# Kernel tuning notes

Hardware: AMD Instinct MI355X
Metric: run time of the kernel (lower is better)

Reference implementation:

```python
import jax, jax.numpy as jnp
import numpy as np

H = 768      # hidden size
F = 3072     # FFN intermediate (4*H)
E = 8        # num experts
K = 2        # top_k
B, S = 2, 2048


def setup_inputs() -> dict:
    key = jax.random.key(0)
    ks = jax.random.split(key, 6)
    scale_in = 1.0 / np.sqrt(H)
    scale_mid = 1.0 / np.sqrt(F)
    return {
        "x": jax.random.normal(ks[0], (B, S, H), dtype=jnp.float32),
        "gate_w": jax.random.normal(ks[1], (H, E), dtype=jnp.float32) * scale_in,
        "W1": jax.random.normal(ks[2], (E, H, F), dtype=jnp.float32) * scale_in,
        "b1": jnp.zeros((E, F), dtype=jnp.float32),
        "W2": jax.random.normal(ks[3], (E, F, H), dtype=jnp.float32) * scale_mid,
        "b2": jnp.zeros((E, H), dtype=jnp.float32),
    }


def reference(x, gate_w, W1, b1, W2, b2):
    """MoE FFN: top-k router -> per-expert FFN -> weighted combine.

    Faithful to the torch module: router logits = x @ gate_w (no bias),
    softmax over the top-k logits only, each expert is a dense FFN
    (Linear -> GELU -> Linear), output = sum_k w_k * expert_{idx_k}(x).
    Expressed densely: combine weights are scattered into a [T, E] matrix
    (zero for unselected experts), so running every expert on every token
    and contracting with the combine matrix yields identical math.
    """
    batch, seq_len, hidden = x.shape
    xf = x.reshape(-1, hidden)                       # [T, H]
    T = xf.shape[0]

    logits = xf @ gate_w                             # [T, E]
    top_w, top_idx = jax.lax.top_k(logits, K)        # [T, K]
    top_w = jax.nn.softmax(top_w, axis=-1)

    # scatter top-k softmax weights into dense [T, E] combine matrix
    comb = jnp.zeros((T, E), dtype=x.dtype).at[
        jnp.arange(T)[:, None], top_idx
    ].add(top_w)

    # all experts on all tokens (zero combine weight kills unselected)
    h = jnp.einsum('th,ehf->etf', xf, W1) + b1[:, None, :]   # [E, T, F]
    h = jax.nn.gelu(h)
    y = jnp.einsum('etf,efh->eth', h, W2) + b2[:, None, :]   # [E, T, H]

    out = jnp.einsum('te,eth->th', comb, y)                  # [T, H]
    return out.reshape(batch, seq_len, hidden)
```

## Files before the change

### kernel.cpp

```cpp
#include <hip/hip_runtime.h>

#define H 768
#define F 3072
#define NE 8
#define T 4096
#define NA 8192
#define TP 10240
#define NRB2 40
#define NRB1 80

typedef unsigned short ushort_t;
typedef __attribute__((ext_vector_type(8))) short bfx8;
typedef __attribute__((ext_vector_type(4))) float fx4;
typedef __attribute__((address_space(3))) const ushort_t lus;

__device__ __forceinline__ ushort_t f2bf(float f) {
    union { float f; unsigned u; } v; v.f = f;
    unsigned u = v.u;
    unsigned r = (u + 0x7fffu + ((u >> 16) & 1u)) >> 16;
    return (ushort_t)r;
}

__device__ __forceinline__ float gelu_tanh(float x) {
    const float c = 0.7978845608028654f;
    float z = c * (x + 0.044715f * x * x * x);
    float t = 1.0f - 2.0f / (__expf(2.0f * z) + 1.0f);
    return 0.5f * x * (1.0f + t);
}

__device__ __forceinline__ void g2l16(const void* g, void* l) {
    __builtin_amdgcn_global_load_lds(
        (__attribute__((address_space(1))) void*)g,
        (__attribute__((address_space(3))) void*)l, 16, 0, 0);
}

__device__ __forceinline__ bfx8 dsr128(lus* p) {
    bfx8 r;
    asm volatile("ds_read_b128 %0, %1" : "=v"(r) : "v"(p));
    return r;
}

#define WAITV6 asm volatile("s_waitcnt vmcnt(6)" ::: "memory")
#define WAITV0 asm volatile("s_waitcnt vmcnt(0)" ::: "memory")
#define LGKM8  asm volatile("s_waitcnt lgkmcnt(8)" ::: "memory")
#define LGKM0  asm volatile("s_waitcnt lgkmcnt(0)" ::: "memory")
#define SBAR   asm volatile("s_barrier" ::: "memory")
#define SCHED0 __builtin_amdgcn_sched_barrier(0)
#define PRIO1  __builtin_amdgcn_s_setprio(1)
#define PRIO0  __builtin_amdgcn_s_setprio(0)

__global__ void router_k(const float* __restrict__ x, const float* __restrict__ gw,
                         int* __restrict__ tidx, float* __restrict__ twgt) {
    int t = blockIdx.x * 4 + (threadIdx.x >> 6);
    int lane = threadIdx.x & 63;
    const float* xr = x + (size_t)t * H;
    float acc[NE];
#pragma unroll
    for (int e = 0; e < NE; ++e) acc[e] = 0.f;
    for (int h = lane; h < H; h += 64) {
        float xv = xr[h];
        const float* g = gw + h * NE;
#pragma unroll
        for (int e = 0; e < NE; ++e) acc[e] += xv * g[e];
    }
#pragma unroll
    for (int off = 32; off > 0; off >>= 1) {
#pragma unroll
        for (int e = 0; e < NE; ++e) acc[e] += __shfl_down(acc[e], off);
    }
    if (lane == 0) {
        float l0 = -1e30f, l1 = -1e30f; int i0 = 0, i1 = 0;
#pragma unroll
        for (int e = 0; e < NE; ++e) {
            float v = acc[e];
            if (v > l0) { l1 = l0; i1 = i0; l0 = v; i0 = e; }
            else if (v > l1) { l1 = v; i1 = e; }
        }
        float w0 = 1.f / (1.f + __expf(l1 - l0));
        tidx[t * 2] = i0; tidx[t * 2 + 1] = i1;
        twgt[t * 2] = w0; twgt[t * 2 + 1] = 1.f - w0;
    }
}

__global__ void init_k(int* counts, int* tos) {
    int i = blockIdx.x * 256 + threadIdx.x;
    if (i < NE) counts[i] = 0;
    if (i < TP) tos[i] = -1;
}

__global__ void count_k(const int* __restrict__ tidx, int* counts) {
    int i = blockIdx.x * 256 + threadIdx.x;
    if (i < NA) atomicAdd(&counts[tidx[i]], 1);
}

__global__ void offsets_k(const int* __restrict__ counts, int* cursor,
                          int* rbe2, int* rbs2, int* rbe1, int* rbs1) {
    int off = 0, rb2 = 0, rb1 = 0;
    for (int e = 0; e < NE; ++e) {
        cursor[e] = off;
        int nrb = (counts[e] + 255) / 256;
        for (int j = 0; j < nrb; ++j) {
            rbe2[rb2] = e; rbs2[rb2] = off + j * 256; ++rb2;
            rbe1[rb1] = e; rbs1[rb1] = off + j * 256; ++rb1;
            rbe1[rb1] = e; rbs1[rb1] = off + j * 256 + 128; ++rb1;
        }
        off += nrb * 256;
    }
    for (; rb2 < NRB2; ++rb2) rbe2[rb2] = -1;
    for (; rb1 < NRB1; ++rb1) rbe1[rb1] = -1;
}

__global__ void scatter_k(const int* __restrict__ tidx, int* cursor,
                          int* __restrict__ tos, int* __restrict__ aslot) {
    int i = blockIdx.x * 256 + threadIdx.x;
    if (i < NA) {
        int e = tidx[i];
        int slot = atomicAdd(&cursor[e], 1);
        tos[slot] = i >> 1;
        aslot[i] = slot;
    }
}

__global__ void gather_k(const float* __restrict__ x, const int* __restrict__ tos,
                         ushort_t* __restrict__ xg) {
    int i = blockIdx.x * 256 + threadIdx.x;
    int slot = i / (H / 8);
    int j = i % (H / 8);
    int tok = tos[slot];
    ushort_t v[8];
    if (tok < 0) {
#pragma unroll
        for (int q = 0; q < 8; ++q) v[q] = 0;
    } else {
        const float* src = x + (size_t)tok * H + j * 8;
#pragma unroll
        for (int q = 0; q < 8; ++q) v[q] = f2bf(src[q]);
    }
    *(bfx8*)&xg[(size_t)slot * H + j * 8] = *(const bfx8*)v;
}

__global__ void transpose_cast_k(const float* __restrict__ src, ushort_t* __restrict__ dst,
                                 int R, int C) {
    int e = blockIdx.z;
    src += (size_t)e * R * C;
    dst += (size_t)e * R * C;
    int c0 = blockIdx.x * 64, r0 = blockIdx.y * 64;
    __shared__ float tile[64][65];
    int tid = threadIdx.x;
    int cc = tid & 63, rr = tid >> 6;
#pragma unroll
    for (int rep = 0; rep < 16; ++rep) {
        int r = rep * 4 + rr;
        tile[r][cc] = src[(size_t)(r0 + r) * C + c0 + cc];
    }
    __syncthreads();
#pragma unroll
    for (int rep = 0; rep < 16; ++rep) {
        int c = rep * 4 + rr;
        dst[(size_t)(c0 + c) * R + r0 + cc] = f2bf(tile[cc][c]);
    }
}

template <int WM, int WN, int DO_GELU>
__global__ __launch_bounds__(512, 2)
void gemm_tile_k(const ushort_t* __restrict__ A, const ushort_t* __restrict__ Bt,
                 const float* __restrict__ bias, void* __restrict__ Cout,
                 const int* __restrict__ rbe, const int* __restrict__ rbs,
                 int K, int N, int ncb) {
    constexpr int BM = WM * 64, BN = WN * 64;
    constexpr int UA = BM / 64, UB = BN / 64;
    constexpr int BUFS = (BM + BN) * 64;

    int nwg = gridDim.x, bid = blockIdx.x;
    int wgid = (bid & 7) * (nwg >> 3) + (bid >> 3);
    int rb = wgid / ncb, cb = wgid % ncb;
    int e = rbe[rb];
    if (e < 0) return;
    int slot0 = rbs[rb];

    __shared__ __align__(16) ushort_t lds[3 * BUFS];

    int tid = threadIdx.x, lane = tid & 63, wid = tid >> 6;
    int wm = wid / WN, wn = wid % WN;
    int l15 = lane & 15, qh = lane >> 4, sw = l15 & 7;

    const ushort_t* Ab = A + (size_t)slot0 * K;
    const ushort_t* Bb = Bt + ((size_t)e * N + cb * BN) * K;

    int j = tid >> 3, q = tid & 7;
    int cs = (q ^ (j & 7)) * 8;
    int ldsw = wid * 512;
    const ushort_t* aSrc = Ab + (size_t)j * K + cs;
    const ushort_t* bSrc = Bb + (size_t)j * K + cs;

    int ch0 = ((0 * 4 + qh) ^ sw) << 3;
    int ch1 = ((1 * 4 + qh) ^ sw) << 3;
    int abase = (wm * 64 + l15) * 64;
    int bbase = BM * 64 + (wn * 64 + l15) * 64;

#define STAGE_T(NB, KT) do { \
    _Pragma("unroll") for (int u = 0; u < UA; ++u) \
        g2l16(aSrc + (size_t)u * 64 * K + (KT) * 64, \
              &lds[(NB) * BUFS + u * 4096 + ldsw]); \
    _Pragma("unroll") for (int u = 0; u < UB; ++u) \
        g2l16(bSrc + (size_t)u * 64 * K + (KT) * 64, \
              &lds[(NB) * BUFS + BM * 64 + u * 4096 + ldsw]); \
} while (0)

    fx4 acc[4][4];
#pragma unroll
    for (int m = 0; m < 4; ++m)
#pragma unroll
        for (int n = 0; n < 4; ++n) acc[m][n] = (fx4){0.f, 0.f, 0.f, 0.f};
    bfx8 a0[4], a1[4], b0v[4], b1v[4];

    int NT = K >> 6;
    STAGE_T(0, 0);
    STAGE_T(1, 1);

#define KBODY(NB, SB, TT) do { \
    if ((TT) + 1 < NT) { WAITV6; } else { WAITV0; } \
    SBAR; \
    { \
      int ab = (NB) * BUFS + abase, bb = (NB) * BUFS + bbase; \
      _Pragma("unroll") for (int m = 0; m < 4; ++m) a0[m] = dsr128((lus*)&lds[ab + m * 1024 + ch0]); \
      _Pragma("unroll") for (int n = 0; n < 4; ++n) b0v[n] = dsr128((lus*)&lds[bb + n * 1024 + ch0]); \
      _Pragma("unroll") for (int m = 0; m < 4; ++m) a1[m] = dsr128((lus*)&lds[ab + m * 1024 + ch1]); \
      _Pragma("unroll") for (int n = 0; n < 4; ++n) b1v[n] = dsr128((lus*)&lds[bb + n * 1024 + ch1]); \
    } \
    if ((TT) + 2 < NT) STAGE_T(SB, (TT) + 2); \
    LGKM8; SCHED0; \
    PRIO1; \
    _Pragma("unroll") for (int m = 0; m < 4; ++m) \
    _Pragma("unroll") for (int n = 0; n < 4; ++n) \
        acc[m][n] = __builtin_amdgcn_mfma_f32_16x16x32_bf16(a0[m], b0v[n], acc[m][n], 0, 0, 0); \
    PRIO0; \
    LGKM0; SCHED0; \
    PRIO1; \
    _Pragma("unroll") for (int m = 0; m < 4; ++m) \
    _Pragma("unroll") for (int n = 0; n < 4; ++n) \
        acc[m][n] = __builtin_amdgcn_mfma_f32_16x16x32_bf16(a1[m], b1v[n], acc[m][n], 0, 0, 0); \
    PRIO0; \
} while (0)

    for (int t3 = 0; t3 < NT; t3 += 3) {
        KBODY(0, 2, t3);
        KBODY(1, 0, t3 + 1);
        KBODY(2, 1, t3 + 2);
    }
#undef KBODY
#undef STAGE_T

#pragma unroll
    for (int n = 0; n < 4; ++n) {
        int col = cb * BN + wn * 64 + n * 16 + l15;
        float bvv = bias[(size_t)e * N + col];
#pragma unroll
        for (int m = 0; m < 4; ++m) {
            int rowb = slot0 + wm * 64 + m * 16 + qh * 4;
            fx4 v = acc[m][n];
#pragma unroll
            for (int jj = 0; jj < 4; ++jj) {
                float val = v[jj] + bvv;
                if (DO_GELU) {
                    ((ushort_t*)Cout)[(size_t)(rowb + jj) * N + col] = f2bf(gelu_tanh(val));
                } else {
                    ((float*)Cout)[(size_t)(rowb + jj) * N + col] = val;
                }
            }
        }
    }
}

__global__ void combine_k(const float* __restrict__ y, const int* __restrict__ aslot,
                          const float* __restrict__ twgt, float* __restrict__ out) {
    int i = blockIdx.x * 256 + threadIdx.x;
    int t = i / (H / 4);
    int j = i % (H / 4);
    int s0 = aslot[t * 2], s1 = aslot[t * 2 + 1];
    float w0 = twgt[t * 2], w1 = twgt[t * 2 + 1];
    const float4 a = ((const float4*)(y + (size_t)s0 * H))[j];
    const float4 b = ((const float4*)(y + (size_t)s1 * H))[j];
    float4 r;
    r.x = w0 * a.x + w1 * b.x;
    r.y = w0 * a.y + w1 * b.y;
    r.z = w0 * a.z + w1 * b.z;
    r.w = w0 * a.w + w1 * b.w;
    ((float4*)(out + (size_t)t * H))[j] = r;
}

extern "C" void kernel_launch(void* const* d_in, const int* in_sizes, int n_in,
                              void* d_out, int out_size, void* d_ws, size_t ws_size,
                              hipStream_t stream) {
    const float* x  = (const float*)d_in[0];
    const float* gw = (const float*)d_in[1];
    const float* W1 = (const float*)d_in[2];
    const float* b1 = (const float*)d_in[3];
    const float* W2 = (const float*)d_in[4];
    const float* b2 = (const float*)d_in[5];
    float* out = (float*)d_out;

    char* ws = (char*)d_ws;
    size_t o = 0;
    auto carve = [&](size_t bytes) -> void* {
        o = (o + 255) & ~(size_t)255;
        void* p = ws + o;
        o += bytes;
        return p;
    };
    int*      tidx   = (int*)carve((size_t)NA * 4);
    float*    twgt   = (float*)carve((size_t)NA * 4);
    int*      counts = (int*)carve(NE * 4);
    int*      cursor = (int*)carve(NE * 4);
    int*      rbe2   = (int*)carve(NRB2 * 4);
    int*      rbs2   = (int*)carve(NRB2 * 4);
    int*      rbe1   = (int*)carve(NRB1 * 4);
    int*      rbs1   = (int*)carve(NRB1 * 4);
    int*      aslot  = (int*)carve((size_t)NA * 4);
    int*      tos    = (int*)carve((size_t)TP * 4);
    ushort_t* xg     = (ushort_t*)carve((size_t)TP * H * 2);
    ushort_t* w1t    = (ushort_t*)carve((size_t)NE * H * F * 2);
    ushort_t* w2t    = (ushort_t*)carve((size_t)NE * H * F * 2);
    ushort_t* hbuf   = (ushort_t*)carve((size_t)TP * F * 2);
    float*    ybuf   = (float*)xg;
    (void)in_sizes; (void)n_in; (void)out_size; (void)ws_size;

    hipLaunchKernelGGL(init_k, dim3(TP / 256), dim3(256), 0, stream, counts, tos);
    hipLaunchKernelGGL(router_k, dim3(T / 4), dim3(256), 0, stream, x, gw, tidx, twgt);
    hipLaunchKernelGGL(count_k, dim3(NA / 256), dim3(256), 0, stream, tidx, counts);
    hipLaunchKernelGGL(offsets_k, dim3(1), dim3(1), 0, stream, counts, cursor,
                       rbe2, rbs2, rbe1, rbs1);
    hipLaunchKernelGGL(scatter_k, dim3(NA / 256), dim3(256), 0, stream, tidx, cursor, tos, aslot);
    hipLaunchKernelGGL(gather_k, dim3(TP * (H / 8) / 256), dim3(256), 0, stream, x, tos, xg);
    hipLaunchKernelGGL(transpose_cast_k, dim3(F / 64, H / 64, NE), dim3(256), 0, stream, W1, w1t, H, F);
    hipLaunchKernelGGL(transpose_cast_k, dim3(H / 64, F / 64, NE), dim3(256), 0, stream, W2, w2t, F, H);
    hipLaunchKernelGGL((gemm_tile_k<2, 4, 1>), dim3(NRB1 * (F / 256)), dim3(512), 0, stream,
                       xg, w1t, b1, (void*)hbuf, rbe1, rbs1, H, F, F / 256);
    hipLaunchKernelGGL((gemm_tile_k<4, 2, 0>), dim3(NRB2 * (H / 128)), dim3(512), 0, stream,
                       hbuf, w2t, b2, (void*)ybuf, rbe2, rbs2, F, H, H / 128);
    hipLaunchKernelGGL(combine_k, dim3(T * (H / 4) / 256), dim3(256), 0, stream,
                       ybuf, aslot, twgt, out);
}
```

Before: 259.8 us.

## Switch expert GEMMs to 128x256 tiles, 256-thread blocks, double buffering

```diff
diff --git a/kernel.cpp b/kernel.cpp
--- a/kernel.cpp
+++ b/kernel.cpp
@@ -5,9 +5,8 @@
 #define NE 8
 #define T 4096
 #define NA 8192
-#define TP 10240
-#define NRB2 40
-#define NRB1 80
+#define TP 9216
+#define NRB 72
 
 typedef unsigned short ushort_t;
 typedef __attribute__((ext_vector_type(8))) short bfx8;
@@ -40,14 +39,14 @@
     return r;
 }
 
-#define WAITV6 asm volatile("s_waitcnt vmcnt(6)" ::: "memory")
-#define WAITV0 asm volatile("s_waitcnt vmcnt(0)" ::: "memory")
-#define LGKM8  asm volatile("s_waitcnt lgkmcnt(8)" ::: "memory")
-#define LGKM0  asm volatile("s_waitcnt lgkmcnt(0)" ::: "memory")
-#define SBAR   asm volatile("s_barrier" ::: "memory")
-#define SCHED0 __builtin_amdgcn_sched_barrier(0)
-#define PRIO1  __builtin_amdgcn_s_setprio(1)
-#define PRIO0  __builtin_amdgcn_s_setprio(0)
+#define WAITV12 asm volatile("s_waitcnt vmcnt(12)" ::: "memory")
+#define WAITV0  asm volatile("s_waitcnt vmcnt(0)" ::: "memory")
+#define LGKM12  asm volatile("s_waitcnt lgkmcnt(12)" ::: "memory")
+#define LGKM0   asm volatile("s_waitcnt lgkmcnt(0)" ::: "memory")
+#define SBAR    asm volatile("s_barrier" ::: "memory")
+#define SCHED0  __builtin_amdgcn_sched_barrier(0)
+#define PRIO1   __builtin_amdgcn_s_setprio(1)
+#define PRIO0   __builtin_amdgcn_s_setprio(0)
 
 __global__ void router_k(const float* __restrict__ x, const float* __restrict__ gw,
                          int* __restrict__ tidx, float* __restrict__ twgt) {
@@ -94,20 +93,15 @@
 }
 
 __global__ void offsets_k(const int* __restrict__ counts, int* cursor,
-                          int* rbe2, int* rbs2, int* rbe1, int* rbs1) {
-    int off = 0, rb2 = 0, rb1 = 0;
+                          int* rbe, int* rbs) {
+    int off = 0, rb = 0;
     for (int e = 0; e < NE; ++e) {
         cursor[e] = off;
-        int nrb = (counts[e] + 255) / 256;
-        for (int j = 0; j < nrb; ++j) {
-            rbe2[rb2] = e; rbs2[rb2] = off + j * 256; ++rb2;
-            rbe1[rb1] = e; rbs1[rb1] = off + j * 256; ++rb1;
-            rbe1[rb1] = e; rbs1[rb1] = off + j * 256 + 128; ++rb1;
-        }
-        off += nrb * 256;
-    }
-    for (; rb2 < NRB2; ++rb2) rbe2[rb2] = -1;
-    for (; rb1 < NRB1; ++rb1) rbe1[rb1] = -1;
+        int nrb = (counts[e] + 127) / 128;
+        for (int j = 0; j < nrb; ++j) { rbe[rb] = e; rbs[rb] = off + j * 128; ++rb; }
+        off += nrb * 128;
+    }
+    for (; rb < NRB; ++rb) rbe[rb] = -1;
 }
 
 __global__ void scatter_k(const int* __restrict__ tidx, int* cursor,
@@ -161,16 +155,13 @@
     }
 }
 
-template <int WM, int WN, int DO_GELU>
-__global__ __launch_bounds__(512, 2)
+template <int DO_GELU>
+__global__ __launch_bounds__(256, 1)
 void gemm_tile_k(const ushort_t* __restrict__ A, const ushort_t* __restrict__ Bt,
                  const float* __restrict__ bias, void* __restrict__ Cout,
                  const int* __restrict__ rbe, const int* __restrict__ rbs,
                  int K, int N, int ncb) {
-    constexpr int BM = WM * 64, BN = WN * 64;
-    constexpr int UA = BM / 64, UB = BN / 64;
-    constexpr int BUFS = (BM + BN) * 64;
-
+    constexpr int BUFS = 24576;
     int nwg = gridDim.x, bid = blockIdx.x;
     int wgid = (bid & 7) * (nwg >> 3) + (bid >> 3);
     int rb = wgid / ncb, cb = wgid % ncb;
@@ -178,14 +169,14 @@
     if (e < 0) return;
     int slot0 = rbs[rb];
 
-    __shared__ __align__(16) ushort_t lds[3 * BUFS];
+    __shared__ __align__(16) ushort_t lds[2 * BUFS];
 
     int tid = threadIdx.x, lane = tid & 63, wid = tid >> 6;
-    int wm = wid / WN, wn = wid % WN;
+    int wm = wid >> 1, wn = wid & 1;
     int l15 = lane & 15, qh = lane >> 4, sw = l15 & 7;
 
     const ushort_t* Ab = A + (size_t)slot0 * K;
-    const ushort_t* Bb = Bt + ((size_t)e * N + cb * BN) * K;
+    const ushort_t* Bb = Bt + ((size_t)e * N + cb * 256) * K;
 
     int j = tid >> 3, q = tid & 7;
     int cs = (q ^ (j & 7)) * 8;
@@ -193,67 +184,67 @@
     const ushort_t* aSrc = Ab + (size_t)j * K + cs;
     const ushort_t* bSrc = Bb + (size_t)j * K + cs;
 
-    int ch0 = ((0 * 4 + qh) ^ sw) << 3;
-    int ch1 = ((1 * 4 + qh) ^ sw) << 3;
+    int ch0 = (qh ^ sw) << 3;
+    int ch1 = ((4 + qh) ^ sw) << 3;
     int abase = (wm * 64 + l15) * 64;
-    int bbase = BM * 64 + (wn * 64 + l15) * 64;
-
-#define STAGE_T(NB, KT) do { \
-    _Pragma("unroll") for (int u = 0; u < UA; ++u) \
-        g2l16(aSrc + (size_t)u * 64 * K + (KT) * 64, \
-              &lds[(NB) * BUFS + u * 4096 + ldsw]); \
-    _Pragma("unroll") for (int u = 0; u < UB; ++u) \
-        g2l16(bSrc + (size_t)u * 64 * K + (KT) * 64, \
-              &lds[(NB) * BUFS + BM * 64 + u * 4096 + ldsw]); \
+    int bbase = 8192 + (wn * 128 + l15) * 64;
+
+#define STAGE_T(BUF, KT) do { \
+    _Pragma("unroll") for (int u = 0; u < 4; ++u) \
+        g2l16(aSrc + (size_t)u * 32 * K + (KT) * 64, \
+              &lds[(BUF) * BUFS + u * 2048 + ldsw]); \
+    _Pragma("unroll") for (int u = 0; u < 8; ++u) \
+        g2l16(bSrc + (size_t)u * 32 * K + (KT) * 64, \
+              &lds[(BUF) * BUFS + 8192 + u * 2048 + ldsw]); \
 } while (0)
 
-    fx4 acc[4][4];
+    fx4 acc[4][8];
 #pragma unroll
     for (int m = 0; m < 4; ++m)
 #pragma unroll
-        for (int n = 0; n < 4; ++n) acc[m][n] = (fx4){0.f, 0.f, 0.f, 0.f};
-    bfx8 a0[4], a1[4], b0v[4], b1v[4];
+        for (int n = 0; n < 8; ++n) acc[m][n] = (fx4){0.f, 0.f, 0.f, 0.f};
+    bfx8 a0[4], a1[4], b0v[8], b1v[8];
 
     int NT = K >> 6;
     STAGE_T(0, 0);
     STAGE_T(1, 1);
 
-#define KBODY(NB, SB, TT) do { \
-    if ((TT) + 1 < NT) { WAITV6; } else { WAITV0; } \
+#define KBODY(BUF, TT) do { \
+    if ((TT) + 1 < NT) { WAITV12; } else { WAITV0; } \
     SBAR; \
     { \
-      int ab = (NB) * BUFS + abase, bb = (NB) * BUFS + bbase; \
+      int ab = (BUF) * BUFS + abase, bb = (BUF) * BUFS + bbase; \
       _Pragma("unroll") for (int m = 0; m < 4; ++m) a0[m] = dsr128((lus*)&lds[ab + m * 1024 + ch0]); \
-      _Pragma("unroll") for (int n = 0; n < 4; ++n) b0v[n] = dsr128((lus*)&lds[bb + n * 1024 + ch0]); \
+      _Pragma("unroll") for (int n = 0; n < 8; ++n) b0v[n] = dsr128((lus*)&lds[bb + n * 1024 + ch0]); \
       _Pragma("unroll") for (int m = 0; m < 4; ++m) a1[m] = dsr128((lus*)&lds[ab + m * 1024 + ch1]); \
-      _Pragma("unroll") for (int n = 0; n < 4; ++n) b1v[n] = dsr128((lus*)&lds[bb + n * 1024 + ch1]); \
+      _Pragma("unroll") for (int n = 0; n < 8; ++n) b1v[n] = dsr128((lus*)&lds[bb + n * 1024 + ch1]); \
     } \
-    if ((TT) + 2 < NT) STAGE_T(SB, (TT) + 2); \
-    LGKM8; SCHED0; \
+    LGKM12; SCHED0; \
     PRIO1; \
     _Pragma("unroll") for (int m = 0; m < 4; ++m) \
-    _Pragma("unroll") for (int n = 0; n < 4; ++n) \
+    _Pragma("unroll") for (int n = 0; n < 8; ++n) \
         acc[m][n] = __builtin_amdgcn_mfma_f32_16x16x32_bf16(a0[m], b0v[n], acc[m][n], 0, 0, 0); \
     PRIO0; \
     LGKM0; SCHED0; \
     PRIO1; \
     _Pragma("unroll") for (int m = 0; m < 4; ++m) \
-    _Pragma("unroll") for (int n = 0; n < 4; ++n) \
+    _Pragma("unroll") for (int n = 0; n < 8; ++n) \
         acc[m][n] = __builtin_amdgcn_mfma_f32_16x16x32_bf16(a1[m], b1v[n], acc[m][n], 0, 0, 0); \
     PRIO0; \
+    SBAR; \
+    if ((TT) + 2 < NT) STAGE_T(BUF, (TT) + 2); \
 } while (0)
 
-    for (int t3 = 0; t3 < NT; t3 += 3) {
-        KBODY(0, 2, t3);
-        KBODY(1, 0, t3 + 1);
-        KBODY(2, 1, t3 + 2);
+    for (int t = 0; t < NT; t += 2) {
+        KBODY(0, t);
+        KBODY(1, t + 1);
     }
 #undef KBODY
 #undef STAGE_T
 
 #pragma unroll
-    for (int n = 0; n < 4; ++n) {
-        int col = cb * BN + wn * 64 + n * 16 + l15;
+    for (int n = 0; n < 8; ++n) {
+        int col = cb * 256 + wn * 128 + n * 16 + l15;
         float bvv = bias[(size_t)e * N + col];
 #pragma unroll
         for (int m = 0; m < 4; ++m) {
@@ -312,10 +303,8 @@
     float*    twgt   = (float*)carve((size_t)NA * 4);
     int*      counts = (int*)carve(NE * 4);
     int*      cursor = (int*)carve(NE * 4);
-    int*      rbe2   = (int*)carve(NRB2 * 4);
-    int*      rbs2   = (int*)carve(NRB2 * 4);
-    int*      rbe1   = (int*)carve(NRB1 * 4);
-    int*      rbs1   = (int*)carve(NRB1 * 4);
+    int*      rbe    = (int*)carve(NRB * 4);
+    int*      rbs    = (int*)carve(NRB * 4);
     int*      aslot  = (int*)carve((size_t)NA * 4);
     int*      tos    = (int*)carve((size_t)TP * 4);
     ushort_t* xg     = (ushort_t*)carve((size_t)TP * H * 2);
@@ -328,16 +317,15 @@
     hipLaunchKernelGGL(init_k, dim3(TP / 256), dim3(256), 0, stream, counts, tos);
     hipLaunchKernelGGL(router_k, dim3(T / 4), dim3(256), 0, stream, x, gw, tidx, twgt);
     hipLaunchKernelGGL(count_k, dim3(NA / 256), dim3(256), 0, stream, tidx, counts);
-    hipLaunchKernelGGL(offsets_k, dim3(1), dim3(1), 0, stream, counts, cursor,
-                       rbe2, rbs2, rbe1, rbs1);
+    hipLaunchKernelGGL(offsets_k, dim3(1), dim3(1), 0, stream, counts, cursor, rbe, rbs);
     hipLaunchKernelGGL(scatter_k, dim3(NA / 256), dim3(256), 0, stream, tidx, cursor, tos, aslot);
     hipLaunchKernelGGL(gather_k, dim3(TP * (H / 8) / 256), dim3(256), 0, stream, x, tos, xg);
     hipLaunchKernelGGL(transpose_cast_k, dim3(F / 64, H / 64, NE), dim3(256), 0, stream, W1, w1t, H, F);
     hipLaunchKernelGGL(transpose_cast_k, dim3(H / 64, F / 64, NE), dim3(256), 0, stream, W2, w2t, F, H);
-    hipLaunchKernelGGL((gemm_tile_k<2, 4, 1>), dim3(NRB1 * (F / 256)), dim3(512), 0, stream,
-                       xg, w1t, b1, (void*)hbuf, rbe1, rbs1, H, F, F / 256);
-    hipLaunchKernelGGL((gemm_tile_k<4, 2, 0>), dim3(NRB2 * (H / 128)), dim3(512), 0, stream,
-                       hbuf, w2t, b2, (void*)ybuf, rbe2, rbs2, F, H, H / 128);
+    hipLaunchKernelGGL((gemm_tile_k<1>), dim3(NRB * (F / 256)), dim3(256), 0, stream,
+                       xg, w1t, b1, (void*)hbuf, rbe, rbs, H, F, F / 256);
+    hipLaunchKernelGGL((gemm_tile_k<0>), dim3(NRB * (H / 256)), dim3(256), 0, stream,
+                       hbuf, w2t, b2, (void*)ybuf, rbe, rbs, F, H, H / 256);
     hipLaunchKernelGGL(combine_k, dim3(T * (H / 4) / 256), dim3(256), 0, stream,
                        ybuf, aslot, twgt, out);
 }
```

New measurement: 279.3 us. +7.5%, slower.
